# Kernel optimization log

Hardware: AMD Instinct MI355X
Metric: run time of the kernel (lower is better)

The kernel has to match this reference:

```python
import jax, jax.numpy as jnp
import numpy as np

N_NODES = 50000
N_HEDGES = 10000
N_MEMB = 800000
IN_SIZE = 256
HEADS = 4
OUT_SIZE = 64


def setup_inputs() -> dict:
    key = jax.random.key(0)
    k1, k2, k3, k4, k5 = jax.random.split(key, 5)
    x = jax.random.normal(k1, (N_NODES, IN_SIZE), dtype=jnp.float32)
    # Linear weight stored as [in, out*heads] so projection is x @ W (same math as torch Linear)
    W = jax.random.normal(k2, (IN_SIZE, OUT_SIZE * HEADS), dtype=jnp.float32) * (1.0 / np.sqrt(IN_SIZE))
    att_e = jax.random.normal(k3, (1, HEADS, OUT_SIZE), dtype=jnp.float32) * 0.1
    node_idx = jax.random.randint(k4, (N_MEMB,), 0, N_NODES, dtype=jnp.int64)
    hedge_idx = jax.random.randint(k5, (N_MEMB,), 0, N_HEDGES, dtype=jnp.int64)
    return {"x": x, "W": W, "att_e": att_e, "node_idx": node_idx,
            "hedge_idx": hedge_idx, "num_hyperedges": N_HEDGES}


def reference(x, W, att_e, node_idx, hedge_idx, num_hyperedges):
    # Dropout is treated as eval-mode identity.
    N = x.shape[0]
    H, D = att_e.shape[1], att_e.shape[2]
    xp = (x @ W).reshape(N, H, D)                                   # [N,H,D]
    # Stage 1: mean-aggregate node features into hyperedges (belongs-to)
    ones = jnp.ones(node_idx.shape[0], dtype=x.dtype)
    deg = jax.ops.segment_sum(ones, hedge_idx, num_segments=num_hyperedges)  # [E]
    he = jax.ops.segment_sum(xp[node_idx], hedge_idx, num_segments=num_hyperedges)
    he = he / jnp.maximum(deg, 1.0)[:, None, None]                  # [E,H,D]
    # Attention logit per hyperedge
    alpha_e = jax.nn.leaky_relu(jnp.sum(he * att_e, axis=-1), 0.2)  # [E,H]
    # Stage 2: edge_softmax over 'contains' edges grouped by destination node
    ae = alpha_e[hedge_idx]                                         # [M,H]
    mx = jax.ops.segment_max(ae, node_idx, num_segments=N)          # [N,H]
    ex = jnp.exp(ae - mx[node_idx])
    den = jax.ops.segment_sum(ex, node_idx, num_segments=N)         # [N,H]
    a = ex / den[node_idx]                                          # [M,H]
    # Attention-weighted scatter-sum of hyperedge features to nodes
    out = jax.ops.segment_sum(he[hedge_idx] * a[:, :, None], node_idx, num_segments=N)  # [N,H,D]
    return out.reshape(N, H * D)
```

## Files before the change

kernel.cpp:

```cpp
#include <hip/hip_runtime.h>
#include <hip/hip_fp16.h>
#include <math.h>

#define N_NODES  50000
#define N_HEDGES 10000
#define N_MEMB   800000
#define KIN      256
#define CH       256
#define HEADS    4
#define HCAP     160
#define NCAP     48
#define GR       16

#define NCHUNK      125
#define CHUNK4      1600
#define HIST_BLOCKS (3 * NCHUNK)
#define XCVT_F4     3200000
#define XCVT_BLOCKS 1563
#define WCVT_BLOCKS 8
#define NB_NODE     50000
#define NB_HEDGE    10000
#define NHALF       25000

__device__ inline float2 h2f(unsigned u) {
    __half2 h = __builtin_bit_cast(__half2, u);
    return __half22float2(h);
}
__device__ inline unsigned f2h(float a, float b) {
    return __builtin_bit_cast(unsigned, __floats2half2_rn(a, b));
}
__device__ inline void accU4(float4& A, float4& B, uint4 g) {
    float2 f0 = h2f(g.x), f1 = h2f(g.y), f2 = h2f(g.z), f3 = h2f(g.w);
    A.x += f0.x; A.y += f0.y; A.z += f1.x; A.w += f1.y;
    B.x += f2.x; B.y += f2.y; B.z += f3.x; B.w += f3.y;
}
__device__ inline void fmaU4(float4& A, float4& B, float w, uint4 g) {
    float2 f0 = h2f(g.x), f1 = h2f(g.y), f2 = h2f(g.z), f3 = h2f(g.w);
    A.x += w * f0.x; A.y += w * f0.y; A.z += w * f1.x; A.w += w * f1.y;
    B.x += w * f2.x; B.y += w * f2.y; B.z += w * f3.x; B.w += w * f3.y;
}

__global__ __launch_bounds__(1024)
void k_hist_cvt(const int4* __restrict__ ni4, const int4* __restrict__ hi4,
                unsigned short* __restrict__ htab, unsigned short* __restrict__ ntab,
                const float4* __restrict__ x4, uint2* __restrict__ x16,
                const float4* __restrict__ Wf, uint2* __restrict__ W16) {
    __shared__ unsigned sh[12500];
    int bid = blockIdx.x, tid = threadIdx.x;
    if (bid < HIST_BLOCKS) {
        int phase = bid / NCHUNK, chunk = bid % NCHUNK;
        int words = (phase == 0) ? (NB_HEDGE / 2) : (NHALF / 2);
        for (int i = tid; i < words; i += 1024) sh[i] = 0;
        __syncthreads();
        int base4 = chunk * CHUNK4;
        if (phase == 0) {
            for (int i = tid; i < CHUNK4; i += 1024) {
                int4 e = hi4[base4 + i];
                atomicAdd(&sh[e.x >> 1], (e.x & 1) ? 65536u : 1u);
                atomicAdd(&sh[e.y >> 1], (e.y & 1) ? 65536u : 1u);
                atomicAdd(&sh[e.z >> 1], (e.z & 1) ? 65536u : 1u);
                atomicAdd(&sh[e.w >> 1], (e.w & 1) ? 65536u : 1u);
            }
        } else {
            int lo = (phase == 1) ? 0 : NHALF;
            for (int i = tid; i < CHUNK4; i += 1024) {
                int4 n = ni4[base4 + i];
                int b;
                b = n.x - lo; if ((unsigned)b < NHALF) atomicAdd(&sh[b >> 1], (b & 1) ? 65536u : 1u);
                b = n.y - lo; if ((unsigned)b < NHALF) atomicAdd(&sh[b >> 1], (b & 1) ? 65536u : 1u);
                b = n.z - lo; if ((unsigned)b < NHALF) atomicAdd(&sh[b >> 1], (b & 1) ? 65536u : 1u);
                b = n.w - lo; if ((unsigned)b < NHALF) atomicAdd(&sh[b >> 1], (b & 1) ? 65536u : 1u);
            }
        }
        __syncthreads();
        unsigned* dst = (phase == 0)
            ? (unsigned*)(htab + (size_t)chunk * NB_HEDGE)
            : (unsigned*)(ntab + (size_t)chunk * NB_NODE + (phase == 2 ? NHALF : 0));
        for (int i = tid; i < words; i += 1024) dst[i] = sh[i];
    } else if (bid < HIST_BLOCKS + XCVT_BLOCKS) {
        int i0 = (bid - HIST_BLOCKS) * 2048 + tid;
        #pragma unroll
        for (int r = 0; r < 2; r++) {
            int idx = i0 + r * 1024;
            if (idx < XCVT_F4) {
                float4 v = x4[idx];
                uint2 u; u.x = f2h(v.x, v.y); u.y = f2h(v.z, v.w);
                x16[idx] = u;
            }
        }
    } else {
        int i0 = (bid - HIST_BLOCKS - XCVT_BLOCKS) * 2048 + tid;
        #pragma unroll
        for (int r = 0; r < 2; r++) {
            int idx = i0 + r * 1024;
            float4 v = Wf[idx];
            uint2 u; u.x = f2h(v.x, v.y); u.y = f2h(v.z, v.w);
            W16[idx] = u;
        }
    }
}

__global__ __launch_bounds__(1024)
void k_scan(unsigned short* __restrict__ htab, unsigned short* __restrict__ ntab,
            int* __restrict__ hdeg, int* __restrict__ ndeg) {
    int bid = blockIdx.x, tid = threadIdx.x;
    if (bid < 49) {
        int b = bid * 1024 + tid;
        if (b < NB_NODE) {
            int run = 0;
            for (int c = 0; c < NCHUNK; c++) {
                size_t idx = (size_t)c * NB_NODE + b;
                int v = ntab[idx];
                ntab[idx] = (unsigned short)run;
                run += v;
            }
            ndeg[b] = run;
        }
    } else {
        int b = (bid - 49) * 1024 + tid;
        if (b < NB_HEDGE) {
            int run = 0;
            for (int c = 0; c < NCHUNK; c++) {
                size_t idx = (size_t)c * NB_HEDGE + b;
                int v = htab[idx];
                htab[idx] = (unsigned short)run;
                run += v;
            }
            hdeg[b] = run;
        }
    }
}

__global__ __launch_bounds__(1024)
void k_place(const int4* __restrict__ ni4, const int4* __restrict__ hi4,
             const unsigned short* __restrict__ htab, const unsigned short* __restrict__ ntab,
             int* __restrict__ hmem, int* __restrict__ nhedge) {
    __shared__ unsigned sh[12500];
    int bid = blockIdx.x, tid = threadIdx.x;
    int phase = bid / NCHUNK, chunk = bid % NCHUNK;
    int words = (phase == 0) ? (NB_HEDGE / 2) : (NHALF / 2);
    for (int i = tid; i < words; i += 1024) sh[i] = 0;
    __syncthreads();
    int base4 = chunk * CHUNK4;
    if (phase == 0) {
        const unsigned short* off = htab + (size_t)chunk * NB_HEDGE;
        for (int i = tid; i < CHUNK4; i += 1024) {
            int4 e = hi4[base4 + i]; int4 n = ni4[base4 + i];
            #pragma unroll
            for (int k = 0; k < 4; k++) {
                int b = (&e.x)[k], v = (&n.x)[k];
                unsigned old = atomicAdd(&sh[b >> 1], (b & 1) ? 65536u : 1u);
                int r = (b & 1) ? (int)(old >> 16) : (int)(old & 0xffffu);
                int pos = (int)off[b] + r;
                if (pos < HCAP) hmem[(size_t)b * HCAP + pos] = v;
            }
        }
    } else {
        int lo = (phase == 1) ? 0 : NHALF;
        const unsigned short* off = ntab + (size_t)chunk * NB_NODE;
        for (int i = tid; i < CHUNK4; i += 1024) {
            int4 e = hi4[base4 + i]; int4 n = ni4[base4 + i];
            #pragma unroll
            for (int k = 0; k < 4; k++) {
                int nb = (&n.x)[k], v = (&e.x)[k];
                int b = nb - lo;
                if ((unsigned)b < NHALF) {
                    unsigned old = atomicAdd(&sh[b >> 1], (b & 1) ? 65536u : 1u);
                    int r = (b & 1) ? (int)(old >> 16) : (int)(old & 0xffffu);
                    int pos = (int)off[nb] + r;
                    if (pos < NCAP) nhedge[(size_t)nb * NCAP + pos] = v;
                }
            }
        }
    }
}

__global__ __launch_bounds__(256, 6)
void k_stage1(const int* __restrict__ hdeg, const int* __restrict__ hmem,
              const uint4* __restrict__ x16u4, uint4* __restrict__ hxu4) {
    __shared__ int sidx[4][HCAP];
    int tid = threadIdx.x;
    int w = tid >> 6, L = tid & 63;
    int half = L >> 5, q = L & 31;
    int e = blockIdx.x * 4 + w;
    int deg = hdeg[e];
    int degC = min(deg, HCAP);
    const int* ml = hmem + (size_t)e * HCAP;
    for (int j = L; j < degC; j += 64) sidx[w][j] = ml[j];
    __syncthreads();
    float4 A0 = {0,0,0,0}, B0 = {0,0,0,0}, A1 = {0,0,0,0}, B1 = {0,0,0,0};
    int j = 0;
    for (; j + 16 <= degC; j += 16) {
        uint4 g[8];
        #pragma unroll
        for (int i = 0; i < 8; i++) {
            int m = sidx[w][j + 2 * i + half];
            g[i] = x16u4[(size_t)m * 32 + q];
        }
        #pragma unroll
        for (int i = 0; i < 8; i++) {
            if (i & 1) accU4(A1, B1, g[i]);
            else       accU4(A0, B0, g[i]);
        }
    }
    for (; j < degC; j += 2) {
        int jj = j + half;
        uint4 g = {0, 0, 0, 0};
        if (jj < degC) g = x16u4[(size_t)sidx[w][jj] * 32 + q];
        accU4(A0, B0, g);
    }
    float4 A = make_float4(A0.x + A1.x, A0.y + A1.y, A0.z + A1.z, A0.w + A1.w);
    float4 B = make_float4(B0.x + B1.x, B0.y + B1.y, B0.z + B1.z, B0.w + B1.w);
    A.x += __shfl_xor(A.x, 32, 64); A.y += __shfl_xor(A.y, 32, 64);
    A.z += __shfl_xor(A.z, 32, 64); A.w += __shfl_xor(A.w, 32, 64);
    B.x += __shfl_xor(B.x, 32, 64); B.y += __shfl_xor(B.y, 32, 64);
    B.z += __shfl_xor(B.z, 32, 64); B.w += __shfl_xor(B.w, 32, 64);
    if (half == 0) {
        float inv = deg > 0 ? 1.0f / (float)deg : 0.0f;
        uint4 o;
        o.x = f2h(A.x * inv, A.y * inv); o.y = f2h(A.z * inv, A.w * inv);
        o.z = f2h(B.x * inv, B.y * inv); o.w = f2h(B.z * inv, B.w * inv);
        hxu4[(size_t)e * 32 + q] = o;
    }
}

__global__ void k_gemm_alpha(const uint2* __restrict__ hx, const __half* __restrict__ W16,
                             const float* __restrict__ att, __half* __restrict__ he,
                             float* __restrict__ alpha) {
    __shared__ float xs[GR][KIN];
    int tid = threadIdx.x;
    int e0 = blockIdx.x * GR;
    #pragma unroll
    for (int jj = 0; jj < GR * 64 / 256; jj++) {
        int f = jj * 256 + tid;
        int r = f >> 6, k4 = f & 63;
        uint2 u = hx[(size_t)(e0 + r) * 64 + k4];
        float2 lo = h2f(u.x), hi = h2f(u.y);
        *(float4*)&xs[r][k4 * 4] = make_float4(lo.x, lo.y, hi.x, hi.y);
    }
    __syncthreads();
    float acc[GR];
    #pragma unroll
    for (int r = 0; r < GR; r++) acc[r] = 0.f;
    int c = tid;
    const __half* wp = W16 + c;
    for (int k = 0; k < KIN; k++) {
        float wv = __half2float(wp[(size_t)k * CH]);
        #pragma unroll
        for (int r = 0; r < GR; r++) acc[r] += xs[r][k] * wv;
    }
    #pragma unroll
    for (int r = 0; r < GR; r++)
        he[(size_t)(e0 + r) * CH + c] = __float2half_rn(acc[r]);
    float av = att[c];
    int lane = tid & 63, h = tid >> 6;
    #pragma unroll
    for (int r = 0; r < GR; r++) {
        float p = acc[r] * av;
        #pragma unroll
        for (int d = 32; d >= 1; d >>= 1) p += __shfl_xor(p, d, 64);
        if (lane == 0) alpha[(e0 + r) * HEADS + h] = p > 0.f ? p : 0.2f * p;
    }
}

__global__ __launch_bounds__(256, 6)
void k_stage2(const uint4* __restrict__ heu4, const float4* __restrict__ alpha4,
              const int* __restrict__ ndeg, const int* __restrict__ nhedge,
              float4* __restrict__ out) {
    __shared__ int   nh[4][NCAP];
    __shared__ float wl[4][4][NCAP];
    int tid = threadIdx.x;
    int w = tid >> 6, L = tid & 63;
    int half = L >> 5, q = L & 31;
    int n = blockIdx.x * 4 + w;
    int deg = min(ndeg[n], NCAP);
    const int* nl = nhedge + (size_t)n * NCAP;
    if (L < deg) nh[w][L] = nl[L];
    __syncthreads();
    float4 mx = make_float4(-INFINITY, -INFINITY, -INFINITY, -INFINITY);
    float4 w4 = make_float4(0.f, 0.f, 0.f, 0.f);
    float4 aj = mx;
    if (L < deg) { aj = alpha4[nh[w][L]]; mx = aj; }
    #pragma unroll
    for (int d = 32; d >= 1; d >>= 1) {
        mx.x = fmaxf(mx.x, __shfl_xor(mx.x, d, 64));
        mx.y = fmaxf(mx.y, __shfl_xor(mx.y, d, 64));
        mx.z = fmaxf(mx.z, __shfl_xor(mx.z, d, 64));
        mx.w = fmaxf(mx.w, __shfl_xor(mx.w, d, 64));
    }
    if (L < deg) {
        w4.x = __expf(aj.x - mx.x); w4.y = __expf(aj.y - mx.y);
        w4.z = __expf(aj.z - mx.z); w4.w = __expf(aj.w - mx.w);
        wl[w][0][L] = w4.x; wl[w][1][L] = w4.y;
        wl[w][2][L] = w4.z; wl[w][3][L] = w4.w;
    }
    float4 dn = w4;
    #pragma unroll
    for (int d = 32; d >= 1; d >>= 1) {
        dn.x += __shfl_xor(dn.x, d, 64);
        dn.y += __shfl_xor(dn.y, d, 64);
        dn.z += __shfl_xor(dn.z, d, 64);
        dn.w += __shfl_xor(dn.w, d, 64);
    }
    __syncthreads();
    int h = q >> 3;
    float den = h < 2 ? (h == 0 ? dn.x : dn.y) : (h == 2 ? dn.z : dn.w);
    float4 A = make_float4(0.f, 0.f, 0.f, 0.f);
    float4 B = make_float4(0.f, 0.f, 0.f, 0.f);
    int j = 0;
    for (; j + 8 <= deg; j += 8) {
        uint4 g[4]; float wgt[4];
        #pragma unroll
        for (int i = 0; i < 4; i++) {
            int jj = j + 2 * i + half;
            wgt[i] = wl[w][h][jj];
            g[i] = heu4[(size_t)nh[w][jj] * 32 + q];
        }
        #pragma unroll
        for (int i = 0; i < 4; i++) fmaU4(A, B, wgt[i], g[i]);
    }
    for (; j < deg; j += 2) {
        int jj = j + half;
        uint4 g = {0, 0, 0, 0}; float ww = 0.f;
        if (jj < deg) { ww = wl[w][h][jj]; g = heu4[(size_t)nh[w][jj] * 32 + q]; }
        fmaU4(A, B, ww, g);
    }
    A.x += __shfl_xor(A.x, 32, 64); A.y += __shfl_xor(A.y, 32, 64);
    A.z += __shfl_xor(A.z, 32, 64); A.w += __shfl_xor(A.w, 32, 64);
    B.x += __shfl_xor(B.x, 32, 64); B.y += __shfl_xor(B.y, 32, 64);
    B.z += __shfl_xor(B.z, 32, 64); B.w += __shfl_xor(B.w, 32, 64);
    if (half == 0) {
        if (deg > 0) {
            float inv = 1.0f / den;
            A.x *= inv; A.y *= inv; A.z *= inv; A.w *= inv;
            B.x *= inv; B.y *= inv; B.z *= inv; B.w *= inv;
        }
        out[(size_t)n * 64 + 2 * q]     = A;
        out[(size_t)n * 64 + 2 * q + 1] = B;
    }
}

extern "C" void kernel_launch(void* const* d_in, const int* in_sizes, int n_in,
                              void* d_out, int out_size, void* d_ws, size_t ws_size,
                              hipStream_t stream) {
    const float* x        = (const float*)d_in[0];
    const float* W        = (const float*)d_in[1];
    const float* att      = (const float*)d_in[2];
    const int*   node_idx = (const int*)d_in[3];
    const int*   hedge_idx= (const int*)d_in[4];
    float4* out4 = (float4*)d_out;

    char* ws = (char*)d_ws;
    size_t o = 0;
    auto alloc = [&](size_t b) { size_t r = o; o += (b + 255) & ~(size_t)255; return r; };
    uint2* hx    = (uint2*)(ws + alloc(sizeof(__half) * (size_t)N_HEDGES * KIN));
    float* alpha = (float*)(ws + alloc(sizeof(float) * (size_t)N_HEDGES * HEADS));
    uint2* W16   = (uint2*)(ws + alloc(sizeof(__half) * (size_t)KIN * CH));
    int*   hdeg  = (int*)(ws + alloc(sizeof(int) * N_HEDGES));
    int*   ndeg  = (int*)(ws + alloc(sizeof(int) * N_NODES));
    size_t hmem_off = alloc(sizeof(int) * (size_t)N_HEDGES * HCAP);
    int*    hmem = (int*)(ws + hmem_off);
    __half* he   = (__half*)(ws + hmem_off);
    int*   nhedge = (int*)(ws + alloc(sizeof(int) * (size_t)N_NODES * NCAP));
    unsigned short* htab = (unsigned short*)(ws + alloc(sizeof(short) * (size_t)NCHUNK * NB_HEDGE));
    unsigned short* ntab = (unsigned short*)(ws + alloc(sizeof(short) * (size_t)NCHUNK * NB_NODE));
    if (o > ws_size) return;
    uint2* x16 = (uint2*)d_out;

    k_hist_cvt<<<HIST_BLOCKS + XCVT_BLOCKS + WCVT_BLOCKS, 1024, 0, stream>>>(
        (const int4*)node_idx, (const int4*)hedge_idx, htab, ntab,
        (const float4*)x, x16, (const float4*)W, W16);
    k_scan<<<59, 1024, 0, stream>>>(htab, ntab, hdeg, ndeg);
    k_place<<<HIST_BLOCKS, 1024, 0, stream>>>(
        (const int4*)node_idx, (const int4*)hedge_idx, htab, ntab, hmem, nhedge);
    k_stage1<<<N_HEDGES / 4, 256, 0, stream>>>(hdeg, hmem, (const uint4*)x16, (uint4*)hx);
    k_gemm_alpha<<<N_HEDGES / GR, 256, 0, stream>>>(hx, (const __half*)W16, att, he, alpha);
    k_stage2<<<N_NODES / 4, 256, 0, stream>>>((const uint4*)he, (const float4*)alpha,
                                              ndeg, nhedge, out4);
}
```

Baseline: 194.6 us.

## Sub-bin hyperedge member lists by node range to sort members by node

Splits each hyperedge's counting-sort bin into 13 sub-bins keyed on node index high bits, so each hyperedge's member list comes out roughly sorted by node id. The intent is better gather locality in stage1, where x rows are read per member. To do this it adds a second scan kernel, more histogram phases (6 hedge phases over 130k bins instead of 1), and fewer, larger chunks. The extra histogram and placement work and the added kernel launch could outweigh the locality benefit.

Result: slower. 209.6 us (+7.7%).

```diff
diff --git a/kernel.cpp b/kernel.cpp
--- a/kernel.cpp
+++ b/kernel.cpp
@@ -12,15 +12,20 @@
 #define NCAP     48
 #define GR       16
 
-#define NCHUNK      125
-#define CHUNK4      1600
-#define HIST_BLOCKS (3 * NCHUNK)
+#define NCHUNK   50
+#define CHUNK4   4000
+#define NR       13
+#define RSH      12
+#define BH       (N_HEDGES * NR)
+#define BPP      25000
+#define HPH      6
+#define NPH      2
+#define TOTPH    (HPH + NPH)
+#define HIST_BLOCKS (TOTPH * NCHUNK)
 #define XCVT_F4     3200000
 #define XCVT_BLOCKS 1563
 #define WCVT_BLOCKS 8
 #define NB_NODE     50000
-#define NB_HEDGE    10000
-#define NHALF       25000
 
 __device__ inline float2 h2f(unsigned u) {
     __half2 h = __builtin_bit_cast(__half2, u);
@@ -49,34 +54,37 @@
     int bid = blockIdx.x, tid = threadIdx.x;
     if (bid < HIST_BLOCKS) {
         int phase = bid / NCHUNK, chunk = bid % NCHUNK;
-        int words = (phase == 0) ? (NB_HEDGE / 2) : (NHALF / 2);
-        for (int i = tid; i < words; i += 1024) sh[i] = 0;
+        for (int i = tid; i < 12500; i += 1024) sh[i] = 0;
         __syncthreads();
         int base4 = chunk * CHUNK4;
-        if (phase == 0) {
+        if (phase < HPH) {
+            int lo = phase * BPP;
             for (int i = tid; i < CHUNK4; i += 1024) {
-                int4 e = hi4[base4 + i];
-                atomicAdd(&sh[e.x >> 1], (e.x & 1) ? 65536u : 1u);
-                atomicAdd(&sh[e.y >> 1], (e.y & 1) ? 65536u : 1u);
-                atomicAdd(&sh[e.z >> 1], (e.z & 1) ? 65536u : 1u);
-                atomicAdd(&sh[e.w >> 1], (e.w & 1) ? 65536u : 1u);
+                int4 e = hi4[base4 + i]; int4 n = ni4[base4 + i];
+                #pragma unroll
+                for (int k = 0; k < 4; k++) {
+                    int b = (&e.x)[k] * NR + ((&n.x)[k] >> RSH) - lo;
+                    if ((unsigned)b < BPP) atomicAdd(&sh[b >> 1], (b & 1) ? 65536u : 1u);
+                }
             }
+            __syncthreads();
+            int cnt = min(BPP, BH - lo);
+            unsigned* dst = (unsigned*)(htab + (size_t)chunk * BH + lo);
+            for (int i = tid; i < cnt / 2; i += 1024) dst[i] = sh[i];
         } else {
-            int lo = (phase == 1) ? 0 : NHALF;
+            int lo = (phase - HPH) * BPP;
             for (int i = tid; i < CHUNK4; i += 1024) {
                 int4 n = ni4[base4 + i];
-                int b;
-                b = n.x - lo; if ((unsigned)b < NHALF) atomicAdd(&sh[b >> 1], (b & 1) ? 65536u : 1u);
-                b = n.y - lo; if ((unsigned)b < NHALF) atomicAdd(&sh[b >> 1], (b & 1) ? 65536u : 1u);
-                b = n.z - lo; if ((unsigned)b < NHALF) atomicAdd(&sh[b >> 1], (b & 1) ? 65536u : 1u);
-                b = n.w - lo; if ((unsigned)b < NHALF) atomicAdd(&sh[b >> 1], (b & 1) ? 65536u : 1u);
+                #pragma unroll
+                for (int k = 0; k < 4; k++) {
+                    int b = (&n.x)[k] - lo;
+                    if ((unsigned)b < BPP) atomicAdd(&sh[b >> 1], (b & 1) ? 65536u : 1u);
+                }
             }
-        }
-        __syncthreads();
-        unsigned* dst = (phase == 0)
-            ? (unsigned*)(htab + (size_t)chunk * NB_HEDGE)
-            : (unsigned*)(ntab + (size_t)chunk * NB_NODE + (phase == 2 ? NHALF : 0));
-        for (int i = tid; i < words; i += 1024) dst[i] = sh[i];
+            __syncthreads();
+            unsigned* dst = (unsigned*)(ntab + (size_t)chunk * NB_NODE + lo);
+            for (int i = tid; i < BPP / 2; i += 1024) dst[i] = sh[i];
+        }
     } else if (bid < HIST_BLOCKS + XCVT_BLOCKS) {
         int i0 = (bid - HIST_BLOCKS) * 2048 + tid;
         #pragma unroll
@@ -102,73 +110,89 @@
 
 __global__ __launch_bounds__(1024)
 void k_scan(unsigned short* __restrict__ htab, unsigned short* __restrict__ ntab,
-            int* __restrict__ hdeg, int* __restrict__ ndeg) {
-    int bid = blockIdx.x, tid = threadIdx.x;
-    if (bid < 49) {
-        int b = bid * 1024 + tid;
-        if (b < NB_NODE) {
-            int run = 0;
-            for (int c = 0; c < NCHUNK; c++) {
-                size_t idx = (size_t)c * NB_NODE + b;
-                int v = ntab[idx];
-                ntab[idx] = (unsigned short)run;
-                run += v;
-            }
-            ndeg[b] = run;
-        }
-    } else {
-        int b = (bid - 49) * 1024 + tid;
-        if (b < NB_HEDGE) {
-            int run = 0;
-            for (int c = 0; c < NCHUNK; c++) {
-                size_t idx = (size_t)c * NB_HEDGE + b;
-                int v = htab[idx];
-                htab[idx] = (unsigned short)run;
-                run += v;
-            }
-            hdeg[b] = run;
-        }
+            int* __restrict__ binTot, int* __restrict__ ndeg) {
+    int b = blockIdx.x * 1024 + threadIdx.x;
+    if (b < BH) {
+        int run = 0;
+        for (int c = 0; c < NCHUNK; c++) {
+            size_t idx = (size_t)c * BH + b;
+            int v = htab[idx];
+            htab[idx] = (unsigned short)run;
+            run += v;
+        }
+        binTot[b] = run;
+    } else if (b < BH + NB_NODE) {
+        int nb = b - BH;
+        int run = 0;
+        for (int c = 0; c < NCHUNK; c++) {
+            size_t idx = (size_t)c * NB_NODE + nb;
+            int v = ntab[idx];
+            ntab[idx] = (unsigned short)run;
+            run += v;
+        }
+        ndeg[nb] = run;
+    }
+}
+
+__global__ __launch_bounds__(1024)
+void k_scan2(const int* __restrict__ binTot, int* __restrict__ rbase,
+             int* __restrict__ hdeg) {
+    int e = blockIdx.x * 1024 + threadIdx.x;
+    if (e < N_HEDGES) {
+        int run = 0;
+        #pragma unroll
+        for (int r = 0; r < NR; r++) {
+            int t = binTot[e * NR + r];
+            rbase[e * NR + r] = run;
+            run += t;
+        }
+        hdeg[e] = run;
     }
 }
 
 __global__ __launch_bounds__(1024)
 void k_place(const int4* __restrict__ ni4, const int4* __restrict__ hi4,
              const unsigned short* __restrict__ htab, const unsigned short* __restrict__ ntab,
+             const int* __restrict__ rbase,
              int* __restrict__ hmem, int* __restrict__ nhedge) {
     __shared__ unsigned sh[12500];
     int bid = blockIdx.x, tid = threadIdx.x;
     int phase = bid / NCHUNK, chunk = bid % NCHUNK;
-    int words = (phase == 0) ? (NB_HEDGE / 2) : (NHALF / 2);
-    for (int i = tid; i < words; i += 1024) sh[i] = 0;
+    for (int i = tid; i < 12500; i += 1024) sh[i] = 0;
     __syncthreads();
     int base4 = chunk * CHUNK4;
-    if (phase == 0) {
-        const unsigned short* off = htab + (size_t)chunk * NB_HEDGE;
+    if (phase < HPH) {
+        int lo = phase * BPP;
+        const unsigned short* off = htab + (size_t)chunk * BH;
         for (int i = tid; i < CHUNK4; i += 1024) {
             int4 e = hi4[base4 + i]; int4 n = ni4[base4 + i];
             #pragma unroll
             for (int k = 0; k < 4; k++) {
-                int b = (&e.x)[k], v = (&n.x)[k];
-                unsigned old = atomicAdd(&sh[b >> 1], (b & 1) ? 65536u : 1u);
-                int r = (b & 1) ? (int)(old >> 16) : (int)(old & 0xffffu);
-                int pos = (int)off[b] + r;
-                if (pos < HCAP) hmem[(size_t)b * HCAP + pos] = v;
+                int ev = (&e.x)[k], nv = (&n.x)[k];
+                int bg = ev * NR + (nv >> RSH);
+                int b = bg - lo;
+                if ((unsigned)b < BPP) {
+                    unsigned old = atomicAdd(&sh[b >> 1], (b & 1) ? 65536u : 1u);
+                    int r = (b & 1) ? (int)(old >> 16) : (int)(old & 0xffffu);
+                    int pos = rbase[bg] + (int)off[bg] + r;
+                    if (pos < HCAP) hmem[(size_t)ev * HCAP + pos] = nv;
+                }
             }
         }
     } else {
-        int lo = (phase == 1) ? 0 : NHALF;
+        int lo = (phase - HPH) * BPP;
         const unsigned short* off = ntab + (size_t)chunk * NB_NODE;
         for (int i = tid; i < CHUNK4; i += 1024) {
             int4 e = hi4[base4 + i]; int4 n = ni4[base4 + i];
             #pragma unroll
             for (int k = 0; k < 4; k++) {
-                int nb = (&n.x)[k], v = (&e.x)[k];
-                int b = nb - lo;
-                if ((unsigned)b < NHALF) {
+                int nv = (&n.x)[k], ev = (&e.x)[k];
+                int b = nv - lo;
+                if ((unsigned)b < BPP) {
                     unsigned old = atomicAdd(&sh[b >> 1], (b & 1) ? 65536u : 1u);
                     int r = (b & 1) ? (int)(old >> 16) : (int)(old & 0xffffu);
-                    int pos = (int)off[nb] + r;
-                    if (pos < NCAP) nhedge[(size_t)nb * NCAP + pos] = v;
+                    int pos = (int)off[nv] + r;
+                    if (pos < NCAP) nhedge[(size_t)nv * NCAP + pos] = ev;
                 }
             }
         }
@@ -358,11 +382,13 @@
     uint2* W16   = (uint2*)(ws + alloc(sizeof(__half) * (size_t)KIN * CH));
     int*   hdeg  = (int*)(ws + alloc(sizeof(int) * N_HEDGES));
     int*   ndeg  = (int*)(ws + alloc(sizeof(int) * N_NODES));
+    int*   binTot= (int*)(ws + alloc(sizeof(int) * BH));
+    int*   rbase = (int*)(ws + alloc(sizeof(int) * BH));
     size_t hmem_off = alloc(sizeof(int) * (size_t)N_HEDGES * HCAP);
     int*    hmem = (int*)(ws + hmem_off);
     __half* he   = (__half*)(ws + hmem_off);
     int*   nhedge = (int*)(ws + alloc(sizeof(int) * (size_t)N_NODES * NCAP));
-    unsigned short* htab = (unsigned short*)(ws + alloc(sizeof(short) * (size_t)NCHUNK * NB_HEDGE));
+    unsigned short* htab = (unsigned short*)(ws + alloc(sizeof(short) * (size_t)NCHUNK * BH));
     unsigned short* ntab = (unsigned short*)(ws + alloc(sizeof(short) * (size_t)NCHUNK * NB_NODE));
     if (o > ws_size) return;
     uint2* x16 = (uint2*)d_out;
@@ -370,9 +396,10 @@
     k_hist_cvt<<<HIST_BLOCKS + XCVT_BLOCKS + WCVT_BLOCKS, 1024, 0, stream>>>(
         (const int4*)node_idx, (const int4*)hedge_idx, htab, ntab,
         (const float4*)x, x16, (const float4*)W, W16);
-    k_scan<<<59, 1024, 0, stream>>>(htab, ntab, hdeg, ndeg);
+    k_scan<<<(BH + NB_NODE + 1023) / 1024, 1024, 0, stream>>>(htab, ntab, binTot, ndeg);
+    k_scan2<<<(N_HEDGES + 1023) / 1024, 1024, 0, stream>>>(binTot, rbase, hdeg);
     k_place<<<HIST_BLOCKS, 1024, 0, stream>>>(
-        (const int4*)node_idx, (const int4*)hedge_idx, htab, ntab, hmem, nhedge);
+        (const int4*)node_idx, (const int4*)hedge_idx, htab, ntab, rbase, hmem, nhedge);
     k_stage1<<<N_HEDGES / 4, 256, 0, stream>>>(hdeg, hmem, (const uint4*)x16, (uint4*)hx);
     k_gemm_alpha<<<N_HEDGES / GR, 256, 0, stream>>>(hx, (const __half*)W16, att, he, alpha);
     k_stage2<<<N_NODES / 4, 256, 0, stream>>>((const uint4*)he, (const float4*)alpha,
```

## Slice fp16 features into 64-byte column slabs for cache-local gathers

Applied to the files above, without the earlier changes.

The fp16 copy of x and the hyperedge feature table are re-laid out as eight column slices, each holding 32 features per row. The stage-1 and stage-2 gather kernels now assign one slice per block, chosen by the low bits of the block id, with 16 lanes-groups of 4 threads each reading 64-byte pieces. The aim is to shrink each block's working set so random gathers hit L2 and MALL more often. The cost is eight times more blocks, each redoing index loads and softmax statistics, plus extra shuffle reductions.

Result: slower. 321.2 us (+65.1%).

```diff
diff --git a/kernel.cpp b/kernel.cpp
--- a/kernel.cpp
+++ b/kernel.cpp
@@ -15,8 +15,8 @@
 #define NCHUNK      125
 #define CHUNK4      1600
 #define HIST_BLOCKS (3 * NCHUNK)
-#define XCVT_F4     3200000
-#define XCVT_BLOCKS 1563
+#define XCVT_U4     1600000
+#define XCVT_BLOCKS 782
 #define WCVT_BLOCKS 8
 #define NB_NODE     50000
 #define NB_HEDGE    10000
@@ -43,7 +43,7 @@
 __global__ __launch_bounds__(1024)
 void k_hist_cvt(const int4* __restrict__ ni4, const int4* __restrict__ hi4,
                 unsigned short* __restrict__ htab, unsigned short* __restrict__ ntab,
-                const float4* __restrict__ x4, uint2* __restrict__ x16,
+                const float4* __restrict__ x4, uint4* __restrict__ x16s,
                 const float4* __restrict__ Wf, uint2* __restrict__ W16) {
     __shared__ unsigned sh[12500];
     int bid = blockIdx.x, tid = threadIdx.x;
@@ -81,11 +81,14 @@
         int i0 = (bid - HIST_BLOCKS) * 2048 + tid;
         #pragma unroll
         for (int r = 0; r < 2; r++) {
-            int idx = i0 + r * 1024;
-            if (idx < XCVT_F4) {
-                float4 v = x4[idx];
-                uint2 u; u.x = f2h(v.x, v.y); u.y = f2h(v.z, v.w);
-                x16[idx] = u;
+            int idx2 = i0 + r * 1024;
+            if (idx2 < XCVT_U4) {
+                int node = idx2 >> 5, q8 = idx2 & 31;
+                float4 v0 = x4[idx2 * 2], v1 = x4[idx2 * 2 + 1];
+                uint4 u;
+                u.x = f2h(v0.x, v0.y); u.y = f2h(v0.z, v0.w);
+                u.z = f2h(v1.x, v1.y); u.w = f2h(v1.z, v1.w);
+                x16s[((size_t)(q8 >> 2) * N_NODES + node) * 4 + (q8 & 3)] = u;
             }
         }
     } else {
@@ -175,57 +178,49 @@
     }
 }
 
-__global__ __launch_bounds__(256, 6)
+__global__ __launch_bounds__(512, 4)
 void k_stage1(const int* __restrict__ hdeg, const int* __restrict__ hmem,
-              const uint4* __restrict__ x16u4, uint4* __restrict__ hxu4) {
-    __shared__ int sidx[4][HCAP];
+              const uint4* __restrict__ x16s, uint4* __restrict__ hx) {
+    __shared__ int sidx[8][HCAP];
     int tid = threadIdx.x;
     int w = tid >> 6, L = tid & 63;
-    int half = L >> 5, q = L & 31;
-    int e = blockIdx.x * 4 + w;
+    int bid = blockIdx.x;
+    int s = bid & 7, g = bid >> 3;
+    int e = g * 8 + w;
+    int q = L & 3, jg = L >> 2;
     int deg = hdeg[e];
     int degC = min(deg, HCAP);
     const int* ml = hmem + (size_t)e * HCAP;
     for (int j = L; j < degC; j += 64) sidx[w][j] = ml[j];
     __syncthreads();
-    float4 A0 = {0,0,0,0}, B0 = {0,0,0,0}, A1 = {0,0,0,0}, B1 = {0,0,0,0};
-    int j = 0;
-    for (; j + 16 <= degC; j += 16) {
-        uint4 g[8];
-        #pragma unroll
-        for (int i = 0; i < 8; i++) {
-            int m = sidx[w][j + 2 * i + half];
-            g[i] = x16u4[(size_t)m * 32 + q];
-        }
-        #pragma unroll
-        for (int i = 0; i < 8; i++) {
-            if (i & 1) accU4(A1, B1, g[i]);
-            else       accU4(A0, B0, g[i]);
-        }
-    }
-    for (; j < degC; j += 2) {
-        int jj = j + half;
-        uint4 g = {0, 0, 0, 0};
-        if (jj < degC) g = x16u4[(size_t)sidx[w][jj] * 32 + q];
-        accU4(A0, B0, g);
-    }
-    float4 A = make_float4(A0.x + A1.x, A0.y + A1.y, A0.z + A1.z, A0.w + A1.w);
-    float4 B = make_float4(B0.x + B1.x, B0.y + B1.y, B0.z + B1.z, B0.w + B1.w);
-    A.x += __shfl_xor(A.x, 32, 64); A.y += __shfl_xor(A.y, 32, 64);
-    A.z += __shfl_xor(A.z, 32, 64); A.w += __shfl_xor(A.w, 32, 64);
-    B.x += __shfl_xor(B.x, 32, 64); B.y += __shfl_xor(B.y, 32, 64);
-    B.z += __shfl_xor(B.z, 32, 64); B.w += __shfl_xor(B.w, 32, 64);
-    if (half == 0) {
+    const uint4* xs = x16s + (size_t)s * N_NODES * 4;
+    float4 A = {0,0,0,0}, B = {0,0,0,0};
+    for (int j0 = 0; j0 < degC; j0 += 32) {
+        int j1 = j0 + jg, j2 = j0 + 16 + jg;
+        uint4 g1 = {0,0,0,0}, g2 = {0,0,0,0};
+        if (j1 < degC) g1 = xs[(size_t)sidx[w][j1] * 4 + q];
+        if (j2 < degC) g2 = xs[(size_t)sidx[w][j2] * 4 + q];
+        accU4(A, B, g1);
+        accU4(A, B, g2);
+    }
+    #pragma unroll
+    for (int d = 4; d <= 32; d <<= 1) {
+        A.x += __shfl_xor(A.x, d, 64); A.y += __shfl_xor(A.y, d, 64);
+        A.z += __shfl_xor(A.z, d, 64); A.w += __shfl_xor(A.w, d, 64);
+        B.x += __shfl_xor(B.x, d, 64); B.y += __shfl_xor(B.y, d, 64);
+        B.z += __shfl_xor(B.z, d, 64); B.w += __shfl_xor(B.w, d, 64);
+    }
+    if (jg == 0) {
         float inv = deg > 0 ? 1.0f / (float)deg : 0.0f;
         uint4 o;
         o.x = f2h(A.x * inv, A.y * inv); o.y = f2h(A.z * inv, A.w * inv);
         o.z = f2h(B.x * inv, B.y * inv); o.w = f2h(B.z * inv, B.w * inv);
-        hxu4[(size_t)e * 32 + q] = o;
+        hx[(size_t)e * 32 + s * 4 + q] = o;
     }
 }
 
 __global__ void k_gemm_alpha(const uint2* __restrict__ hx, const __half* __restrict__ W16,
-                             const float* __restrict__ att, __half* __restrict__ he,
+                             const float* __restrict__ att, __half* __restrict__ he_s,
                              float* __restrict__ alpha) {
     __shared__ float xs[GR][KIN];
     int tid = threadIdx.x;
@@ -249,9 +244,10 @@
         #pragma unroll
         for (int r = 0; r < GR; r++) acc[r] += xs[r][k] * wv;
     }
+    int sl = c >> 5, cs = c & 31;
     #pragma unroll
     for (int r = 0; r < GR; r++)
-        he[(size_t)(e0 + r) * CH + c] = __float2half_rn(acc[r]);
+        he_s[((size_t)sl * N_HEDGES + (e0 + r)) * 32 + cs] = __float2half_rn(acc[r]);
     float av = att[c];
     int lane = tid & 63, h = tid >> 6;
     #pragma unroll
@@ -263,80 +259,59 @@
     }
 }
 
-__global__ __launch_bounds__(256, 6)
-void k_stage2(const uint4* __restrict__ heu4, const float4* __restrict__ alpha4,
+__global__ __launch_bounds__(512, 4)
+void k_stage2(const uint4* __restrict__ he_s, const float* __restrict__ alpha,
               const int* __restrict__ ndeg, const int* __restrict__ nhedge,
               float4* __restrict__ out) {
-    __shared__ int   nh[4][NCAP];
-    __shared__ float wl[4][4][NCAP];
+    __shared__ int nh[8][NCAP];
     int tid = threadIdx.x;
     int w = tid >> 6, L = tid & 63;
-    int half = L >> 5, q = L & 31;
-    int n = blockIdx.x * 4 + w;
+    int bid = blockIdx.x;
+    int s = bid & 7, g = bid >> 3;
+    int n = g * 8 + w;
+    int h = s >> 1;
+    int q = L & 3, jg = L >> 2;
     int deg = min(ndeg[n], NCAP);
     const int* nl = nhedge + (size_t)n * NCAP;
-    if (L < deg) nh[w][L] = nl[L];
+    for (int j = L; j < deg; j += 64) nh[w][j] = nl[j];
     __syncthreads();
-    float4 mx = make_float4(-INFINITY, -INFINITY, -INFINITY, -INFINITY);
-    float4 w4 = make_float4(0.f, 0.f, 0.f, 0.f);
-    float4 aj = mx;
-    if (L < deg) { aj = alpha4[nh[w][L]]; mx = aj; }
-    #pragma unroll
-    for (int d = 32; d >= 1; d >>= 1) {
-        mx.x = fmaxf(mx.x, __shfl_xor(mx.x, d, 64));
-        mx.y = fmaxf(mx.y, __shfl_xor(mx.y, d, 64));
-        mx.z = fmaxf(mx.z, __shfl_xor(mx.z, d, 64));
-        mx.w = fmaxf(mx.w, __shfl_xor(mx.w, d, 64));
-    }
-    if (L < deg) {
-        w4.x = __expf(aj.x - mx.x); w4.y = __expf(aj.y - mx.y);
-        w4.z = __expf(aj.z - mx.z); w4.w = __expf(aj.w - mx.w);
-        wl[w][0][L] = w4.x; wl[w][1][L] = w4.y;
-        wl[w][2][L] = w4.z; wl[w][3][L] = w4.w;
-    }
-    float4 dn = w4;
-    #pragma unroll
-    for (int d = 32; d >= 1; d >>= 1) {
-        dn.x += __shfl_xor(dn.x, d, 64);
-        dn.y += __shfl_xor(dn.y, d, 64);
-        dn.z += __shfl_xor(dn.z, d, 64);
-        dn.w += __shfl_xor(dn.w, d, 64);
-    }
-    __syncthreads();
-    int h = q >> 3;
-    float den = h < 2 ? (h == 0 ? dn.x : dn.y) : (h == 2 ? dn.z : dn.w);
-    float4 A = make_float4(0.f, 0.f, 0.f, 0.f);
-    float4 B = make_float4(0.f, 0.f, 0.f, 0.f);
-    int j = 0;
-    for (; j + 8 <= deg; j += 8) {
-        uint4 g[4]; float wgt[4];
-        #pragma unroll
-        for (int i = 0; i < 4; i++) {
-            int jj = j + 2 * i + half;
-            wgt[i] = wl[w][h][jj];
-            g[i] = heu4[(size_t)nh[w][jj] * 32 + q];
-        }
-        #pragma unroll
-        for (int i = 0; i < 4; i++) fmaU4(A, B, wgt[i], g[i]);
-    }
-    for (; j < deg; j += 2) {
-        int jj = j + half;
-        uint4 g = {0, 0, 0, 0}; float ww = 0.f;
-        if (jj < deg) { ww = wl[w][h][jj]; g = heu4[(size_t)nh[w][jj] * 32 + q]; }
-        fmaU4(A, B, ww, g);
-    }
-    A.x += __shfl_xor(A.x, 32, 64); A.y += __shfl_xor(A.y, 32, 64);
-    A.z += __shfl_xor(A.z, 32, 64); A.w += __shfl_xor(A.w, 32, 64);
-    B.x += __shfl_xor(B.x, 32, 64); B.y += __shfl_xor(B.y, 32, 64);
-    B.z += __shfl_xor(B.z, 32, 64); B.w += __shfl_xor(B.w, 32, 64);
-    if (half == 0) {
-        if (deg > 0) {
-            float inv = 1.0f / den;
-            A.x *= inv; A.y *= inv; A.z *= inv; A.w *= inv;
-            B.x *= inv; B.y *= inv; B.z *= inv; B.w *= inv;
-        }
-        out[(size_t)n * 64 + 2 * q]     = A;
-        out[(size_t)n * 64 + 2 * q + 1] = B;
+    size_t obase = (size_t)n * 64 + s * 8 + q * 2;
+    if (deg == 0) {
+        if (jg == 0) {
+            out[obase]     = make_float4(0.f, 0.f, 0.f, 0.f);
+            out[obase + 1] = make_float4(0.f, 0.f, 0.f, 0.f);
+        }
+        return;
+    }
+    int j0 = jg, j1 = 16 + jg, j2 = 32 + jg;
+    float av0 = -INFINITY, av1 = -INFINITY, av2 = -INFINITY;
+    int e0i = 0, e1i = 0, e2i = 0;
+    if (j0 < deg) { e0i = nh[w][j0]; av0 = alpha[e0i * HEADS + h]; }
+    if (j1 < deg) { e1i = nh[w][j1]; av1 = alpha[e1i * HEADS + h]; }
+    if (j2 < deg) { e2i = nh[w][j2]; av2 = alpha[e2i * HEADS + h]; }
+    float mx = fmaxf(av0, fmaxf(av1, av2));
+    #pragma unroll
+    for (int d = 4; d <= 32; d <<= 1) mx = fmaxf(mx, __shfl_xor(mx, d, 64));
+    float x0 = __expf(av0 - mx), x1 = __expf(av1 - mx), x2 = __expf(av2 - mx);
+    float den = x0 + x1 + x2;
+    #pragma unroll
+    for (int d = 4; d <= 32; d <<= 1) den += __shfl_xor(den, d, 64);
+    const uint4* hs = he_s + (size_t)s * N_HEDGES * 4;
+    float4 A = {0,0,0,0}, B = {0,0,0,0};
+    if (j0 < deg) fmaU4(A, B, x0, hs[(size_t)e0i * 4 + q]);
+    if (j1 < deg) fmaU4(A, B, x1, hs[(size_t)e1i * 4 + q]);
+    if (j2 < deg) fmaU4(A, B, x2, hs[(size_t)e2i * 4 + q]);
+    #pragma unroll
+    for (int d = 4; d <= 32; d <<= 1) {
+        A.x += __shfl_xor(A.x, d, 64); A.y += __shfl_xor(A.y, d, 64);
+        A.z += __shfl_xor(A.z, d, 64); A.w += __shfl_xor(A.w, d, 64);
+        B.x += __shfl_xor(B.x, d, 64); B.y += __shfl_xor(B.y, d, 64);
+        B.z += __shfl_xor(B.z, d, 64); B.w += __shfl_xor(B.w, d, 64);
+    }
+    if (jg == 0) {
+        float inv = 1.0f / den;
+        out[obase]     = make_float4(A.x * inv, A.y * inv, A.z * inv, A.w * inv);
+        out[obase + 1] = make_float4(B.x * inv, B.y * inv, B.z * inv, B.w * inv);
     }
 }
 
@@ -360,21 +335,21 @@
     int*   ndeg  = (int*)(ws + alloc(sizeof(int) * N_NODES));
     size_t hmem_off = alloc(sizeof(int) * (size_t)N_HEDGES * HCAP);
     int*    hmem = (int*)(ws + hmem_off);
-    __half* he   = (__half*)(ws + hmem_off);
+    __half* he_s = (__half*)(ws + hmem_off);
     int*   nhedge = (int*)(ws + alloc(sizeof(int) * (size_t)N_NODES * NCAP));
     unsigned short* htab = (unsigned short*)(ws + alloc(sizeof(short) * (size_t)NCHUNK * NB_HEDGE));
     unsigned short* ntab = (unsigned short*)(ws + alloc(sizeof(short) * (size_t)NCHUNK * NB_NODE));
     if (o > ws_size) return;
-    uint2* x16 = (uint2*)d_out;
+    uint4* x16s = (uint4*)d_out;
 
     k_hist_cvt<<<HIST_BLOCKS + XCVT_BLOCKS + WCVT_BLOCKS, 1024, 0, stream>>>(
         (const int4*)node_idx, (const int4*)hedge_idx, htab, ntab,
-        (const float4*)x, x16, (const float4*)W, W16);
+        (const float4*)x, x16s, (const float4*)W, W16);
     k_scan<<<59, 1024, 0, stream>>>(htab, ntab, hdeg, ndeg);
     k_place<<<HIST_BLOCKS, 1024, 0, stream>>>(
         (const int4*)node_idx, (const int4*)hedge_idx, htab, ntab, hmem, nhedge);
-    k_stage1<<<N_HEDGES / 4, 256, 0, stream>>>(hdeg, hmem, (const uint4*)x16, (uint4*)hx);
-    k_gemm_alpha<<<N_HEDGES / GR, 256, 0, stream>>>(hx, (const __half*)W16, att, he, alpha);
-    k_stage2<<<N_NODES / 4, 256, 0, stream>>>((const uint4*)he, (const float4*)alpha,
-                                              ndeg, nhedge, out4);
-}
+    k_stage1<<<(N_HEDGES / 8) * 8, 512, 0, stream>>>(hdeg, hmem, (const uint4*)x16s, (uint4*)hx);
+    k_gemm_alpha<<<N_HEDGES / GR, 256, 0, stream>>>(hx, (const __half*)W16, att, he_s, alpha);
+    k_stage2<<<(N_NODES / 8) * 8, 512, 0, stream>>>((const uint4*)he_s, alpha,
+                                                    ndeg, nhedge, out4);
+}
```
